# Kernel tuning notes

Measured on AMD Instinct MI355X. Metric: run time of the kernel, lower is better.

Reference implementation:

```python
import jax, jax.numpy as jnp
import numpy as np

N_CELLS = 131072
IN_D, HID_D, OUT_D = 64, 128, 64


def setup_inputs() -> dict:
    key = jax.random.key(0)
    ks = jax.random.split(key, 16)
    rn = lambda k, shape, s=1.0: jax.random.normal(k, shape, dtype=jnp.float32) * s
    return {
        "x": rn(ks[0], (1, IN_D)),
        "hiddens": rn(ks[1], (N_CELLS, HID_D), 0.1),
        # engine_a: Linear(192->128), Linear(128->64)  (torch weight layout [out,in])
        "W1a": rn(ks[2], (128, IN_D + HID_D), 0.1), "b1a": rn(ks[3], (128,), 0.1),
        "W2a": rn(ks[4], (OUT_D, 128), 0.1), "b2a": rn(ks[5], (OUT_D,), 0.1),
        # engine_g: same shapes
        "W1g": rn(ks[6], (128, IN_D + HID_D), 0.1), "b1g": rn(ks[7], (128,), 0.1),
        "W2g": rn(ks[8], (OUT_D, 128), 0.1), "b2g": rn(ks[9], (OUT_D,), 0.1),
        # GRUCell(input=OUT_D+1, hidden=HID_D)
        "Wih": rn(ks[10], (3 * HID_D, OUT_D + 1), 0.1), "Whh": rn(ks[11], (3 * HID_D, HID_D), 0.1),
        "bih": rn(ks[12], (3 * HID_D,), 0.1), "bhh": rn(ks[13], (3 * HID_D,), 0.1),
        # output_head: Linear(OUT_D -> IN_D)
        "Wo": rn(ks[14], (IN_D, OUT_D), 0.1), "bo": rn(ks[15], (IN_D,), 0.1),
        "step": 6,
    }


def gru_cell(inp, h, Wih, Whh, bih, bhh):
    gi = inp @ Wih.T + bih          # [N, 3H]
    gh = h @ Whh.T + bhh            # [N, 3H]
    ir, iz, i_n = jnp.split(gi, 3, axis=-1)
    hr, hz, h_n = jnp.split(gh, 3, axis=-1)
    r = jax.nn.sigmoid(ir + hr)
    z = jax.nn.sigmoid(iz + hz)
    n = jnp.tanh(i_n + r * h_n)
    return (1.0 - z) * n + z * h


def faction_sync(h, nf=8, sync=0.15, debate=0.15, step=0):
    n, d = h.shape
    nf = min(nf, n // 2)
    if nf < 2:
        return h
    fs = n // nf
    hf = h[: nf * fs].reshape(nf, fs, d)
    fm = hf.mean(axis=1, keepdims=True)             # per-faction mean
    hf = (1.0 - sync) * hf + sync * fm
    if step > 5:
        ops = hf.mean(axis=1)                       # [nf, d]
        go = ops.mean(axis=0)                       # [d] global opinion
        dc = max(1, fs // 4)
        hf = hf.at[:, :dc].set((1.0 - debate) * hf[:, :dc] + debate * go)
    return h.at[: nf * fs].set(hf.reshape(nf * fs, d))


def reference(x, hiddens, W1a, b1a, W2a, b2a, W1g, b1g, W2g, b2g,
              Wih, Whh, bih, bhh, Wo, bo, step):
    N = hiddens.shape[0]
    # all cells share the same x; batch the per-cell loop
    c = jnp.concatenate([jnp.broadcast_to(x, (N, x.shape[-1])), hiddens], axis=-1)  # [N,192]
    a = jax.nn.relu(c @ W1a.T + b1a) @ W2a.T + b2a   # [N, OUT_D]
    g = jax.nn.relu(c @ W1g.T + b1g) @ W2g.T + b2g   # [N, OUT_D]
    out = a - g                                      # [N, OUT_D]
    t = jnp.mean(out ** 2, axis=-1)                  # [N] per-cell tension
    # GRU inputs are detached in the original
    gru_in = jax.lax.stop_gradient(jnp.concatenate([out, t[:, None]], axis=-1))  # [N, OUT_D+1]
    new_h = gru_cell(gru_in, hiddens, Wih, Whh, bih, bhh)
    new_h = jax.lax.stop_gradient(new_h)             # .detach() on stacked hiddens
    new_h = faction_sync(new_h, step=int(step))
    # softmax weights built from .item() scalars -> constants w.r.t. grad
    w = jax.nn.softmax(jax.lax.stop_gradient(t))     # [N]
    combined = w @ out                               # [OUT_D]
    pred = (combined @ Wo.T + bo)[None, :]           # [1, IN_D]
    return pred, t.mean(), new_h
```

## Files before the change

### kernel.cpp

```cpp
#include <hip/hip_runtime.h>
#include <math.h>

#define NCELLS 131072
#define IND 64
#define HD 128
#define OUTD 64
#define NF 8
#define FS 16384
#define DC 4096
#define TB 64
#define NBLK (NCELLS/TB)
#define NTH 512
#define NREP 4
#define NT (NCELLS*HD)

typedef __bf16 bf16x8 __attribute__((ext_vector_type(8)));
typedef float f32x4 __attribute__((ext_vector_type(4)));
typedef unsigned short us8 __attribute__((ext_vector_type(8)));

#define MFMA(a,b,c) __builtin_amdgcn_mfma_f32_16x16x32_bf16(a,b,c,0,0,0)

#define WS_W1H 0
#define WS_W2F 32768
#define WS_WIH 49152
#define WS_WHH 73728
#define WS_U_TOTAL 122880
#define WF_B1   0
#define WF_B2   256
#define WF_WT   320
#define WF_FSUM 704
#define WF_WSUM 4800
#define WF_SE   5056
#define WF_TS   5060
#define WF_TOTAL 5064
#define WS_NH_OFF 266240

#define L_SC    0
#define L_SH1   8704
#define L_SOF_F 4352
#define L_SOB   17408
#define L_ST_F  11008
#define L_SE_F  11072
#define L_WSCR_F 11136
#define L_TOT   25600

__device__ __forceinline__ unsigned short f2bf(float f) {
    unsigned u = __builtin_bit_cast(unsigned, f);
    return (unsigned short)((u + 0x7FFFu + ((u >> 16) & 1u)) >> 16);
}
__device__ __forceinline__ float bf2f(unsigned short h) {
    return __builtin_bit_cast(float, (unsigned)h << 16);
}
__device__ __forceinline__ bf16x8 ld8(const unsigned short* p) {
    return __builtin_bit_cast(bf16x8, *(const us8*)p);
}
__device__ __forceinline__ float sigm(float v) {
    return __builtin_amdgcn_rcpf(1.f + __builtin_amdgcn_exp2f(-1.44269504f * v));
}
__device__ __forceinline__ float tanh_fast(float v) {
    return 1.f - 2.f * __builtin_amdgcn_rcpf(1.f + __builtin_amdgcn_exp2f(2.88539008f * v));
}

__global__ __launch_bounds__(256) void convert_kernel(
    const float* __restrict__ x,
    const float* __restrict__ W1a, const float* __restrict__ b1a,
    const float* __restrict__ W2a, const float* __restrict__ b2a,
    const float* __restrict__ W1g, const float* __restrict__ b1g,
    const float* __restrict__ W2g, const float* __restrict__ b2g,
    const float* __restrict__ Wih, const float* __restrict__ Whh,
    unsigned short* __restrict__ wsu, float* __restrict__ wsf)
{
    int i = blockIdx.x * 256 + threadIdx.x;
    if (i < 32768) {
        int frag = i >> 9, r = i & 511;
        int lane = r >> 3, e = r & 7;
        int col = (frag >> 2)*16 + (lane & 15);
        int k   = (frag & 3)*32 + (lane >> 4)*8 + e;
        float v = (col < 128) ? W1a[col*192 + 64 + k] : W1g[(col-128)*192 + 64 + k];
        wsu[WS_W1H + i] = f2bf(v); return;
    }
    int j = i - 32768;
    if (j < 16384) {
        int frag = j >> 9, r = j & 511;
        int lane = r >> 3, e = r & 7;
        int col = (frag >> 3)*16 + (lane & 15);
        int k   = (frag & 7)*32 + (lane >> 4)*8 + e;
        float v = (k < 128) ? W2a[col*128 + k] : -W2g[col*128 + (k-128)];
        wsu[WS_W2F + j] = f2bf(v); return;
    }
    j -= 16384;
    if (j < 24576) {
        int frag = j >> 9, r = j & 511;
        int lane = r >> 3, e = r & 7;
        int col = (frag >> 1)*16 + (lane & 15);
        int k   = (frag & 1)*32 + (lane >> 4)*8 + e;
        wsu[WS_WIH + j] = f2bf(Wih[col*65 + k]); return;
    }
    j -= 24576;
    if (j < 49152) {
        int frag = j >> 9, r = j & 511;
        int lane = r >> 3, e = r & 7;
        int col = (frag >> 2)*16 + (lane & 15);
        int k   = (frag & 3)*32 + (lane >> 4)*8 + e;
        wsu[WS_WHH + j] = f2bf(Whh[col*128 + k]); return;
    }
    j -= 49152;
    if (j < 256) {
        const float* wr = (j < 128) ? (W1a + j*192) : (W1g + (size_t)(j-128)*192);
        float base = (j < 128) ? b1a[j] : b1g[j-128];
        float dot = 0.f;
        #pragma unroll 8
        for (int k = 0; k < 64; ++k) dot += x[k] * wr[k];
        wsf[WF_B1 + j] = base + dot; return;
    }
    j -= 256;
    if (j < 64)  { wsf[WF_B2 + j] = b2a[j] - b2g[j]; return; }
    j -= 64;
    if (j < 384) { wsf[WF_WT + j] = Wih[j*65 + 64]; return; }
}

__global__ __launch_bounds__(NTH, 4) void fused_cell_kernel(
    const float* __restrict__ hiddens,
    const float* __restrict__ bih, const float* __restrict__ bhh,
    const unsigned short* __restrict__ wsu, const float* __restrict__ wsf,
    float* __restrict__ newh, float* __restrict__ fsum,
    float* __restrict__ wsum, float* __restrict__ sumexp, float* __restrict__ tsum,
    int shifted)
{
    __shared__ __align__(16) unsigned short sm[L_TOT];
    float* smf = (float*)sm;

    const int tid = threadIdx.x;
    const int cell0 = blockIdx.x * TB;
    const int w = tid >> 6, lane = tid & 63;
    const int q = lane >> 4, cL = lane & 15;
    const int rep = blockIdx.x & (NREP-1);

    bf16x8 pB1[8];
    {
        const unsigned short* wp = wsu + WS_W1H + (w*2)*4*512 + lane*8;
        #pragma unroll
        for (int k = 0; k < 8; ++k) pB1[k] = ld8(wp + k*512);
    }

    for (int idx = tid; idx < TB*(HD/4); idx += NTH) {
        int c = idx >> 5, k4 = idx & 31;
        float4 v = ((const float4*)hiddens)[(size_t)(cell0+c)*(HD/4) + k4];
        unsigned p0 = (unsigned)f2bf(v.x) | ((unsigned)f2bf(v.y) << 16);
        unsigned p1 = (unsigned)f2bf(v.z) | ((unsigned)f2bf(v.w) << 16);
        *(unsigned*)&sm[L_SC + c*136 + k4*4]     = p0;
        *(unsigned*)&sm[L_SC + c*136 + k4*4 + 2] = p1;
    }
    __syncthreads();

    bf16x8 pB2[8];
    {
        const unsigned short* wp = wsu + WS_W2F + (w & 3)*8*512 + lane*8;
        #pragma unroll
        for (int k = 0; k < 8; ++k) pB2[k] = ld8(wp + k*512);
    }
    #pragma unroll
    for (int ct = 0; ct < 2; ++ct) {
        const int col = w*32 + ct*16 + cL;
        const float bias = wsf[WF_B1 + col];
        f32x4 acc[4];
        #pragma unroll
        for (int m = 0; m < 4; ++m) acc[m] = (f32x4){bias,bias,bias,bias};
        #pragma unroll
        for (int k = 0; k < 4; ++k) {
            bf16x8 B = pB1[ct*4 + k];
            #pragma unroll
            for (int m = 0; m < 4; ++m) {
                bf16x8 A = ld8(&sm[L_SC + (m*16+cL)*136 + k*32 + q*8]);
                acc[m] = MFMA(A, B, acc[m]);
            }
        }
        #pragma unroll
        for (int m = 0; m < 4; ++m)
            #pragma unroll
            for (int r = 0; r < 4; ++r)
                sm[L_SH1 + (m*16+q*4+r)*264 + col] = f2bf(fmaxf(acc[m][r], 0.f));
    }
    __syncthreads();

    bf16x8 pGi[6];
    {
        const unsigned short* wiB = wsu + WS_WIH + lane*8;
        #pragma unroll
        for (int k = 0; k < 2; ++k) {
            pGi[k]   = ld8(wiB + ((     w)*2 + k)*512);
            pGi[2+k] = ld8(wiB + (( 8 + w)*2 + k)*512);
            pGi[4+k] = ld8(wiB + ((16 + w)*2 + k)*512);
        }
    }
    f32x4 o0, o1;
    {
        const int Mt0 = (w >> 2)*2, Mt1 = Mt0 + 1;
        const float bias = wsf[WF_B2 + (w & 3)*16 + cL];
        o0 = (f32x4){bias,bias,bias,bias}; o1 = o0;
        #pragma unroll
        for (int k = 0; k < 8; ++k) {
            bf16x8 B  = pB2[k];
            bf16x8 A0 = ld8(&sm[L_SH1 + (Mt0*16+cL)*264 + k*32 + q*8]);
            o0 = MFMA(A0, B, o0);
            bf16x8 A1 = ld8(&sm[L_SH1 + (Mt1*16+cL)*264 + k*32 + q*8]);
            o1 = MFMA(A1, B, o1);
        }
    }
    __syncthreads();

    {
        const int col = (w & 3)*16 + cL;
        const int Mt0 = (w >> 2)*2, Mt1 = Mt0 + 1;
        #pragma unroll
        for (int r = 0; r < 4; ++r) {
            int r0 = Mt0*16 + q*4 + r, r1 = Mt1*16 + q*4 + r;
            smf[L_SOF_F + r0*68 + col] = o0[r];
            sm [L_SOB   + r0*72 + col] = f2bf(o0[r]);
            smf[L_SOF_F + r1*68 + col] = o1[r];
            sm [L_SOB   + r1*72 + col] = f2bf(o1[r]);
        }
    }
    __syncthreads();

    {
        const int c = tid >> 3, g = tid & 7;
        f32x4 a = *(const f32x4*)&smf[L_SOF_F + c*68 + g*8];
        f32x4 b = *(const f32x4*)&smf[L_SOF_F + c*68 + g*8 + 4];
        float s = a[0]*a[0] + a[1]*a[1] + a[2]*a[2] + a[3]*a[3]
                + b[0]*b[0] + b[1]*b[1] + b[2]*b[2] + b[3]*b[3];
        s += __shfl_xor(s, 1);
        s += __shfl_xor(s, 2);
        s += __shfl_xor(s, 4);
        if (g == 0) {
            float t = s * (1.0f/OUTD);
            smf[L_ST_F + c] = t;
            smf[L_SE_F + c] = __builtin_amdgcn_exp2f(t * 1.44269504f);
        }
    }
    __syncthreads();

    const int fidx = (int)(blockIdx.x >> 8);
    {
        const int j = w*16 + cL;
        const float bR = bih[j]      + bhh[j];
        const float bZ = bih[HD+j]   + bhh[HD+j];
        const float bI = bih[2*HD+j];
        const float bH = bhh[2*HD+j];
        const float wtR = wsf[WF_WT + j];
        const float wtZ = wsf[WF_WT + HD + j];
        const float wtI = wsf[WF_WT + 2*HD + j];
        f32x4 R[4], Z[4], I[4], H[4];
        #pragma unroll
        for (int m = 0; m < 4; ++m) {
            R[m] = (f32x4){bR,bR,bR,bR}; Z[m] = (f32x4){bZ,bZ,bZ,bZ};
            I[m] = (f32x4){bI,bI,bI,bI}; H[m] = (f32x4){bH,bH,bH,bH};
        }
        #pragma unroll
        for (int k = 0; k < 2; ++k) {
            bf16x8 Br = pGi[k], Bz = pGi[2+k], Bi = pGi[4+k];
            #pragma unroll
            for (int m = 0; m < 4; ++m) {
                bf16x8 A = ld8(&sm[L_SOB + (m*16+cL)*72 + k*32 + q*8]);
                R[m] = MFMA(A, Br, R[m]);
                Z[m] = MFMA(A, Bz, Z[m]);
                I[m] = MFMA(A, Bi, I[m]);
            }
        }
        const unsigned short* whB = wsu + WS_WHH + lane*8;
        #pragma unroll
        for (int k = 0; k < 4; ++k) {
            bf16x8 Br = ld8(whB + ((     w)*4 + k)*512);
            bf16x8 Bz = ld8(whB + (( 8 + w)*4 + k)*512);
            bf16x8 Bn = ld8(whB + ((16 + w)*4 + k)*512);
            #pragma unroll
            for (int m = 0; m < 4; ++m) {
                bf16x8 A = ld8(&sm[L_SC + (m*16+cL)*136 + k*32 + q*8]);
                R[m] = MFMA(A, Br, R[m]);
                Z[m] = MFMA(A, Bz, Z[m]);
                H[m] = MFMA(A, Bn, H[m]);
            }
        }
        float colsum = 0.f;
        #pragma unroll
        for (int m = 0; m < 4; ++m) {
            #pragma unroll
            for (int r = 0; r < 4; ++r) {
                const int row = m*16 + q*4 + r;
                const float tv = smf[L_ST_F + row];
                const float rr = sigm(R[m][r] + tv*wtR);
                const float zz = sigm(Z[m][r] + tv*wtZ);
                const float nn = tanh_fast(I[m][r] + tv*wtI + rr*H[m][r]);
                const float hold = bf2f(sm[L_SC + row*136 + j]);
                const float hv = (1.f - zz)*nn + zz*hold;
                int g = (cell0+row)*HD + j;
                int s = g - 3;
                if (g < 3) s = NT - 3 + g;
                if (!shifted) s = g;
                newh[s] = hv;
                colsum += hv;
            }
        }
        colsum += __shfl_xor(colsum, 16);
        colsum += __shfl_xor(colsum, 32);
        if (q == 0) unsafeAtomicAdd(&fsum[(rep*NF + fidx)*HD + j], colsum);
    }

    {
        const int col = tid & 63, cg = tid >> 6;
        float wacc = 0.f;
        #pragma unroll
        for (int c8 = 0; c8 < 8; ++c8) {
            const int c = cg*8 + c8;
            wacc += smf[L_SE_F + c] * smf[L_SOF_F + c*68 + col];
        }
        smf[L_WSCR_F + cg*64 + col] = wacc;
    }
    __syncthreads();
    if (tid < 64) {
        float wacc = 0.f;
        #pragma unroll
        for (int g = 0; g < 8; ++g) wacc += smf[L_WSCR_F + g*64 + tid];
        unsafeAtomicAdd(&wsum[rep*64 + tid], wacc);
        float e = smf[L_SE_F + tid];
        float t = smf[L_ST_F + tid];
        #pragma unroll
        for (int d = 1; d < 64; d <<= 1) { e += __shfl_xor(e, d); t += __shfl_xor(t, d); }
        if (tid == 0) { unsafeAtomicAdd(&sumexp[rep], e); unsafeAtomicAdd(&tsum[rep], t); }
    }
}

#define TBF 64
__global__ __launch_bounds__(256) void faction_kernel(
    const float* __restrict__ src, float* __restrict__ dst,
    const float* __restrict__ fsum, const int* __restrict__ step,
    const float* __restrict__ Wo, const float* __restrict__ bo,
    const float* __restrict__ wsum, const float* __restrict__ sumexp,
    const float* __restrict__ tsum, float* __restrict__ d_out, int shifted)
{
    __shared__ float bnon[HD], bdeb[HD], bnon2[HD], bdeb2[HD];
    const int b = blockIdx.x;
    const int f = b >> 8;
    const int fn = (f + 1 < NF) ? f + 1 : f;
    {
        const int jc = threadIdx.x & 127;
        const int useF = (threadIdx.x < 128) ? f : fn;
        float s = 0.f, fm_s = 0.f;
        #pragma unroll
        for (int rr = 0; rr < NREP; ++rr) {
            #pragma unroll
            for (int ff = 0; ff < NF; ++ff) s += fsum[(rr*NF+ff)*HD + jc];
            fm_s += fsum[(rr*NF+useF)*HD + jc];
        }
        const float go = s * (1.0f/NCELLS);
        const float fm = fm_s * (1.0f/FS);
        if (threadIdx.x < 128) { bnon[jc] = 0.15f*fm;  bdeb[jc] = 0.1275f*fm + 0.15f*go; }
        else                   { bnon2[jc] = 0.15f*fm; bdeb2[jc] = 0.1275f*fm + 0.15f*go; }
    }
    __syncthreads();
    const int sglob = (step[0] > 5) ? 1 : 0;

    if (shifted) {
        const int Fbase = b * 2048;
        #pragma unroll
        for (int it = 0; it < 8; ++it) {
            const int F  = Fbase + threadIdx.x + it*256;
            const int g0 = 4*F + 3;
            float4 v = ((const float4*)src)[F];
            const int c0 = g0 >> 7, j0 = g0 & 127;
            const int d0 = sglob && ((c0 & (FS-1)) < DC);
            const float a0 = d0 ? 0.7225f : 0.85f;
            const float* br0 = d0 ? bdeb : bnon;
            float r0 = a0*v.x + br0[j0], r1, r2, r3;
            if (j0 != 127) {
                r1 = a0*v.y + br0[j0+1];
                r2 = a0*v.z + br0[j0+2];
                r3 = a0*v.w + br0[j0+3];
            } else {
                const int c1 = c0 + 1;
                const int d1 = sglob && ((c1 & (FS-1)) < DC);
                const float a1 = d1 ? 0.7225f : 0.85f;
                const bool nf2 = (c1 >> 14) != f;
                const float* br1 = nf2 ? (d1 ? bdeb2 : bnon2) : (d1 ? bdeb : bnon);
                r1 = a1*v.y + br1[0];
                r2 = a1*v.z + br1[1];
                r3 = a1*v.w + br1[2];
            }
            if (g0 + 3 < NT) {
                float4 o = {r0, r1, r2, r3};
                *(float4*)(dst + g0) = o;
            } else {
                dst[g0] = r0;
            }
        }
        if (b == 0 && threadIdx.x < 3) {
            const int g = threadIdx.x;
            const float a0 = sglob ? 0.7225f : 0.85f;
            const float* br0 = sglob ? bdeb : bnon;
            dst[g] = a0 * src[NT - 3 + g] + br0[g];
        }
    } else {
        const int cell0 = b * TBF;
        const bool debate = sglob && ((cell0 & (FS-1)) < DC);
        const float a = debate ? 0.7225f : 0.85f;
        const float* brow = debate ? bdeb : bnon;
        const float* srow = src + (size_t)cell0*HD;
        float* drow = dst + (size_t)cell0*HD;
        #pragma unroll
        for (int i = 0; i < (TBF*HD)/256; ++i) {
            const int idx = threadIdx.x + i*256;
            drow[idx] = a*srow[idx] + brow[idx & 127];
        }
    }

    if (b == 0 && threadIdx.x < OUTD) {
        const int i = threadIdx.x;
        float seT = 0.f;
        #pragma unroll
        for (int rr = 0; rr < NREP; ++rr) seT += sumexp[rr];
        const float inv = 1.0f / seT;
        const float* wr = Wo + (size_t)i*OUTD;
        float acc = bo[i];
        #pragma unroll 8
        for (int jj = 0; jj < OUTD; ++jj) {
            float wv = wsum[jj] + wsum[64+jj] + wsum[128+jj] + wsum[192+jj];
            acc += (wv*inv) * wr[jj];
        }
        d_out[i] = acc;
        if (i == 0) {
            float tT = 0.f;
            #pragma unroll
            for (int rr = 0; rr < NREP; ++rr) tT += tsum[rr];
            d_out[OUTD] = tT * (1.0f/NCELLS);
        }
    }
}

extern "C" void kernel_launch(void* const* d_in, const int* in_sizes, int n_in,
                              void* d_out, int out_size, void* d_ws, size_t ws_size,
                              hipStream_t stream)
{
    const float* x   = (const float*)d_in[0];
    const float* hid = (const float*)d_in[1];
    const float* W1a = (const float*)d_in[2];
    const float* b1a = (const float*)d_in[3];
    const float* W2a = (const float*)d_in[4];
    const float* b2a = (const float*)d_in[5];
    const float* W1g = (const float*)d_in[6];
    const float* b1g = (const float*)d_in[7];
    const float* W2g = (const float*)d_in[8];
    const float* b2g = (const float*)d_in[9];
    const float* Wih = (const float*)d_in[10];
    const float* Whh = (const float*)d_in[11];
    const float* bih = (const float*)d_in[12];
    const float* bhh = (const float*)d_in[13];
    const float* Wo  = (const float*)d_in[14];
    const float* bo  = (const float*)d_in[15];
    const int*  step = (const int*)d_in[16];

    float* out  = (float*)d_out;
    float* newh_out = out + (OUTD + 1);

    unsigned short* wsu = (unsigned short*)d_ws;
    float* wsf = (float*)(wsu + WS_U_TOTAL);
    float* fsum   = wsf + WF_FSUM;
    float* wsum   = wsf + WF_WSUM;
    float* sumexp = wsf + WF_SE;
    float* tsum   = wsf + WF_TS;

    const size_t need = (size_t)WS_NH_OFF + (size_t)NT*sizeof(float);
    const int shifted = (ws_size >= need) ? 1 : 0;
    float* nh_store = shifted ? (float*)((char*)d_ws + WS_NH_OFF) : newh_out;

    hipMemsetAsync(fsum, 0, (NREP*NF*HD + NREP*OUTD + 2*NREP)*sizeof(float), stream);

    convert_kernel<<<(123584 + 255)/256, 256, 0, stream>>>(
        x, W1a, b1a, W2a, b2a, W1g, b1g, W2g, b2g, Wih, Whh, wsu, wsf);

    fused_cell_kernel<<<NBLK, NTH, 0, stream>>>(
        hid, bih, bhh, wsu, wsf, nh_store, fsum, wsum, sumexp, tsum, shifted);

    faction_kernel<<<NCELLS/TBF, 256, 0, stream>>>(
        nh_store, newh_out, fsum, step, Wo, bo, wsum, sumexp, tsum, out, shifted);
}
```

Baseline: 231.0 us.

## Store intermediate hidden state as fp16 and pad LDS rows to avoid conflicts

The fused cell kernel now writes the pre-sync hidden state to workspace as fp16 instead of fp32, which halves the intermediate write and re-read, and the faction kernel widens it back to fp32. The misaligned shifted-store path is replaced by simple aligned per-row writes. LDS row strides are padded to reduce bank conflicts, the old hidden value for the GRU blend is reloaded in fp32 from global memory rather than from the bf16 copy, and sched barriers are added while occupancy drops to 3 blocks. Rounding the hidden state to fp16 adds precision loss, and the extra global reads of hiddens add traffic.

```diff
diff --git a/kernel.cpp b/kernel.cpp
--- a/kernel.cpp
+++ b/kernel.cpp
@@ -36,20 +36,17 @@
 #define WS_NH_OFF 266240
 
 #define L_SC    0
-#define L_SH1   8704
-#define L_SOF_F 4352
-#define L_SOB   17408
-#define L_ST_F  11008
-#define L_SE_F  11072
-#define L_WSCR_F 11136
-#define L_TOT   25600
+#define L_SH1   8832
+#define L_SOF_F 4416
+#define L_SOB   17536
+#define L_ST_F  12928
+#define L_SE_F  12992
+#define L_WSCR_F 13056
+#define L_TOT   27136
 
 __device__ __forceinline__ unsigned short f2bf(float f) {
     unsigned u = __builtin_bit_cast(unsigned, f);
     return (unsigned short)((u + 0x7FFFu + ((u >> 16) & 1u)) >> 16);
-}
-__device__ __forceinline__ float bf2f(unsigned short h) {
-    return __builtin_bit_cast(float, (unsigned)h << 16);
 }
 __device__ __forceinline__ bf16x8 ld8(const unsigned short* p) {
     return __builtin_bit_cast(bf16x8, *(const us8*)p);
@@ -119,13 +116,13 @@
     if (j < 384) { wsf[WF_WT + j] = Wih[j*65 + 64]; return; }
 }
 
-__global__ __launch_bounds__(NTH, 4) void fused_cell_kernel(
+__global__ __launch_bounds__(NTH, 3) void fused_cell_kernel(
     const float* __restrict__ hiddens,
     const float* __restrict__ bih, const float* __restrict__ bhh,
     const unsigned short* __restrict__ wsu, const float* __restrict__ wsf,
-    float* __restrict__ newh, float* __restrict__ fsum,
-    float* __restrict__ wsum, float* __restrict__ sumexp, float* __restrict__ tsum,
-    int shifted)
+    unsigned short* __restrict__ nh16, float* __restrict__ nhf,
+    float* __restrict__ fsum, float* __restrict__ wsum,
+    float* __restrict__ sumexp, float* __restrict__ tsum, int mode)
 {
     __shared__ __align__(16) unsigned short sm[L_TOT];
     float* smf = (float*)sm;
@@ -142,14 +139,15 @@
         #pragma unroll
         for (int k = 0; k < 8; ++k) pB1[k] = ld8(wp + k*512);
     }
+    __builtin_amdgcn_sched_barrier(0);
 
     for (int idx = tid; idx < TB*(HD/4); idx += NTH) {
         int c = idx >> 5, k4 = idx & 31;
         float4 v = ((const float4*)hiddens)[(size_t)(cell0+c)*(HD/4) + k4];
         unsigned p0 = (unsigned)f2bf(v.x) | ((unsigned)f2bf(v.y) << 16);
         unsigned p1 = (unsigned)f2bf(v.z) | ((unsigned)f2bf(v.w) << 16);
-        *(unsigned*)&sm[L_SC + c*136 + k4*4]     = p0;
-        *(unsigned*)&sm[L_SC + c*136 + k4*4 + 2] = p1;
+        *(unsigned*)&sm[L_SC + c*138 + k4*4]     = p0;
+        *(unsigned*)&sm[L_SC + c*138 + k4*4 + 2] = p1;
     }
     __syncthreads();
 
@@ -159,6 +157,7 @@
         #pragma unroll
         for (int k = 0; k < 8; ++k) pB2[k] = ld8(wp + k*512);
     }
+    __builtin_amdgcn_sched_barrier(0);
     #pragma unroll
     for (int ct = 0; ct < 2; ++ct) {
         const int col = w*32 + ct*16 + cL;
@@ -171,7 +170,7 @@
             bf16x8 B = pB1[ct*4 + k];
             #pragma unroll
             for (int m = 0; m < 4; ++m) {
-                bf16x8 A = ld8(&sm[L_SC + (m*16+cL)*136 + k*32 + q*8]);
+                bf16x8 A = ld8(&sm[L_SC + (m*16+cL)*138 + k*32 + q*8]);
                 acc[m] = MFMA(A, B, acc[m]);
             }
         }
@@ -179,7 +178,7 @@
         for (int m = 0; m < 4; ++m)
             #pragma unroll
             for (int r = 0; r < 4; ++r)
-                sm[L_SH1 + (m*16+q*4+r)*264 + col] = f2bf(fmaxf(acc[m][r], 0.f));
+                sm[L_SH1 + (m*16+q*4+r)*266 + col] = f2bf(fmaxf(acc[m][r], 0.f));
     }
     __syncthreads();
 
@@ -193,6 +192,7 @@
             pGi[4+k] = ld8(wiB + ((16 + w)*2 + k)*512);
         }
     }
+    __builtin_amdgcn_sched_barrier(0);
     f32x4 o0, o1;
     {
         const int Mt0 = (w >> 2)*2, Mt1 = Mt0 + 1;
@@ -201,9 +201,9 @@
         #pragma unroll
         for (int k = 0; k < 8; ++k) {
             bf16x8 B  = pB2[k];
-            bf16x8 A0 = ld8(&sm[L_SH1 + (Mt0*16+cL)*264 + k*32 + q*8]);
+            bf16x8 A0 = ld8(&sm[L_SH1 + (Mt0*16+cL)*266 + k*32 + q*8]);
             o0 = MFMA(A0, B, o0);
-            bf16x8 A1 = ld8(&sm[L_SH1 + (Mt1*16+cL)*264 + k*32 + q*8]);
+            bf16x8 A1 = ld8(&sm[L_SH1 + (Mt1*16+cL)*266 + k*32 + q*8]);
             o1 = MFMA(A1, B, o1);
         }
     }
@@ -256,6 +256,12 @@
             R[m] = (f32x4){bR,bR,bR,bR}; Z[m] = (f32x4){bZ,bZ,bZ,bZ};
             I[m] = (f32x4){bI,bI,bI,bI}; H[m] = (f32x4){bH,bH,bH,bH};
         }
+        float hold[16];
+        #pragma unroll
+        for (int m = 0; m < 4; ++m)
+            #pragma unroll
+            for (int r = 0; r < 4; ++r)
+                hold[m*4+r] = hiddens[(size_t)(cell0 + m*16 + q*4 + r)*HD + j];
         #pragma unroll
         for (int k = 0; k < 2; ++k) {
             bf16x8 Br = pGi[k], Bz = pGi[2+k], Bi = pGi[4+k];
@@ -275,7 +281,7 @@
             bf16x8 Bn = ld8(whB + ((16 + w)*4 + k)*512);
             #pragma unroll
             for (int m = 0; m < 4; ++m) {
-                bf16x8 A = ld8(&sm[L_SC + (m*16+cL)*136 + k*32 + q*8]);
+                bf16x8 A = ld8(&sm[L_SC + (m*16+cL)*138 + k*32 + q*8]);
                 R[m] = MFMA(A, Br, R[m]);
                 Z[m] = MFMA(A, Bz, Z[m]);
                 H[m] = MFMA(A, Bn, H[m]);
@@ -291,13 +297,10 @@
                 const float rr = sigm(R[m][r] + tv*wtR);
                 const float zz = sigm(Z[m][r] + tv*wtZ);
                 const float nn = tanh_fast(I[m][r] + tv*wtI + rr*H[m][r]);
-                const float hold = bf2f(sm[L_SC + row*136 + j]);
-                const float hv = (1.f - zz)*nn + zz*hold;
-                int g = (cell0+row)*HD + j;
-                int s = g - 3;
-                if (g < 3) s = NT - 3 + g;
-                if (!shifted) s = g;
-                newh[s] = hv;
+                const float hv = (1.f - zz)*nn + zz*hold[m*4+r];
+                const size_t g = (size_t)(cell0+row)*HD + j;
+                if (mode) nh16[g] = __builtin_bit_cast(unsigned short, (_Float16)hv);
+                else      nhf[g]  = hv;
                 colsum += hv;
             }
         }
@@ -332,88 +335,56 @@
 
 #define TBF 64
 __global__ __launch_bounds__(256) void faction_kernel(
-    const float* __restrict__ src, float* __restrict__ dst,
+    const unsigned short* __restrict__ src16, float* __restrict__ dst,
     const float* __restrict__ fsum, const int* __restrict__ step,
     const float* __restrict__ Wo, const float* __restrict__ bo,
     const float* __restrict__ wsum, const float* __restrict__ sumexp,
-    const float* __restrict__ tsum, float* __restrict__ d_out, int shifted)
+    const float* __restrict__ tsum, float* __restrict__ d_out, int mode)
 {
-    __shared__ float bnon[HD], bdeb[HD], bnon2[HD], bdeb2[HD];
-    const int b = blockIdx.x;
-    const int f = b >> 8;
-    const int fn = (f + 1 < NF) ? f + 1 : f;
-    {
-        const int jc = threadIdx.x & 127;
-        const int useF = (threadIdx.x < 128) ? f : fn;
+    __shared__ float bnon[HD], bdeb[HD];
+    const int cell0 = blockIdx.x * TBF;
+    const int f = blockIdx.x >> 8;
+    if (threadIdx.x < HD) {
+        const int jc = threadIdx.x;
         float s = 0.f, fm_s = 0.f;
         #pragma unroll
         for (int rr = 0; rr < NREP; ++rr) {
             #pragma unroll
             for (int ff = 0; ff < NF; ++ff) s += fsum[(rr*NF+ff)*HD + jc];
-            fm_s += fsum[(rr*NF+useF)*HD + jc];
+            fm_s += fsum[(rr*NF+f)*HD + jc];
         }
         const float go = s * (1.0f/NCELLS);
         const float fm = fm_s * (1.0f/FS);
-        if (threadIdx.x < 128) { bnon[jc] = 0.15f*fm;  bdeb[jc] = 0.1275f*fm + 0.15f*go; }
-        else                   { bnon2[jc] = 0.15f*fm; bdeb2[jc] = 0.1275f*fm + 0.15f*go; }
-    }
-    __syncthreads();
-    const int sglob = (step[0] > 5) ? 1 : 0;
-
-    if (shifted) {
-        const int Fbase = b * 2048;
-        #pragma unroll
-        for (int it = 0; it < 8; ++it) {
-            const int F  = Fbase + threadIdx.x + it*256;
-            const int g0 = 4*F + 3;
-            float4 v = ((const float4*)src)[F];
-            const int c0 = g0 >> 7, j0 = g0 & 127;
-            const int d0 = sglob && ((c0 & (FS-1)) < DC);
-            const float a0 = d0 ? 0.7225f : 0.85f;
-            const float* br0 = d0 ? bdeb : bnon;
-            float r0 = a0*v.x + br0[j0], r1, r2, r3;
-            if (j0 != 127) {
-                r1 = a0*v.y + br0[j0+1];
-                r2 = a0*v.z + br0[j0+2];
-                r3 = a0*v.w + br0[j0+3];
-            } else {
-                const int c1 = c0 + 1;
-                const int d1 = sglob && ((c1 & (FS-1)) < DC);
-                const float a1 = d1 ? 0.7225f : 0.85f;
-                const bool nf2 = (c1 >> 14) != f;
-                const float* br1 = nf2 ? (d1 ? bdeb2 : bnon2) : (d1 ? bdeb : bnon);
-                r1 = a1*v.y + br1[0];
-                r2 = a1*v.z + br1[1];
-                r3 = a1*v.w + br1[2];
+        bnon[jc] = 0.15f*fm;
+        bdeb[jc] = 0.1275f*fm + 0.15f*go;
+    }
+    __syncthreads();
+    const bool debate = (step[0] > 5) && ((cell0 & (FS-1)) < DC);
+    const float a = debate ? 0.7225f : 0.85f;
+    const float* brow = debate ? bdeb : bnon;
+    float* drow = dst + (size_t)cell0*HD;
+    if (mode) {
+        const unsigned short* srow = src16 + (size_t)cell0*HD;
+        #pragma unroll
+        for (int it = 0; it < 4; ++it) {
+            const int e0 = (threadIdx.x + it*256) * 8;
+            us8 v = *(const us8*)(srow + e0);
+            const int jb = e0 & 127;
+            #pragma unroll
+            for (int u = 0; u < 8; ++u) {
+                float hv = (float)__builtin_bit_cast(_Float16, (unsigned short)v[u]);
+                drow[e0 + u] = a*hv + brow[jb + u];
             }
-            if (g0 + 3 < NT) {
-                float4 o = {r0, r1, r2, r3};
-                *(float4*)(dst + g0) = o;
-            } else {
-                dst[g0] = r0;
-            }
-        }
-        if (b == 0 && threadIdx.x < 3) {
-            const int g = threadIdx.x;
-            const float a0 = sglob ? 0.7225f : 0.85f;
-            const float* br0 = sglob ? bdeb : bnon;
-            dst[g] = a0 * src[NT - 3 + g] + br0[g];
         }
     } else {
-        const int cell0 = b * TBF;
-        const bool debate = sglob && ((cell0 & (FS-1)) < DC);
-        const float a = debate ? 0.7225f : 0.85f;
-        const float* brow = debate ? bdeb : bnon;
-        const float* srow = src + (size_t)cell0*HD;
-        float* drow = dst + (size_t)cell0*HD;
         #pragma unroll
         for (int i = 0; i < (TBF*HD)/256; ++i) {
             const int idx = threadIdx.x + i*256;
-            drow[idx] = a*srow[idx] + brow[idx & 127];
-        }
-    }
-
-    if (b == 0 && threadIdx.x < OUTD) {
+            drow[idx] = a*drow[idx] + brow[idx & 127];
+        }
+    }
+
+    if (blockIdx.x == 0 && threadIdx.x < OUTD) {
         const int i = threadIdx.x;
         float seT = 0.f;
         #pragma unroll
@@ -468,9 +439,9 @@
     float* sumexp = wsf + WF_SE;
     float* tsum   = wsf + WF_TS;
 
-    const size_t need = (size_t)WS_NH_OFF + (size_t)NT*sizeof(float);
-    const int shifted = (ws_size >= need) ? 1 : 0;
-    float* nh_store = shifted ? (float*)((char*)d_ws + WS_NH_OFF) : newh_out;
+    const size_t need = (size_t)WS_NH_OFF + (size_t)NT*sizeof(unsigned short);
+    const int mode = (ws_size >= need) ? 1 : 0;
+    unsigned short* nh16 = (unsigned short*)((char*)d_ws + WS_NH_OFF);
 
     hipMemsetAsync(fsum, 0, (NREP*NF*HD + NREP*OUTD + 2*NREP)*sizeof(float), stream);
 
@@ -478,8 +449,8 @@
         x, W1a, b1a, W2a, b2a, W1g, b1g, W2g, b2g, Wih, Whh, wsu, wsf);
 
     fused_cell_kernel<<<NBLK, NTH, 0, stream>>>(
-        hid, bih, bhh, wsu, wsf, nh_store, fsum, wsum, sumexp, tsum, shifted);
+        hid, bih, bhh, wsu, wsf, nh16, newh_out, fsum, wsum, sumexp, tsum, mode);
 
     faction_kernel<<<NCELLS/TBF, 256, 0, stream>>>(
-        nh_store, newh_out, fsum, step, Wo, bo, wsum, sumexp, tsum, out, shifted);
-}
+        nh16, newh_out, fsum, step, Wo, bo, wsum, sumexp, tsum, out, mode);
+}
```

After: 329.1 us. +42.4%, slower.
